# Kernel optimization log

Measured on AMD Instinct MI355X. Metric: run time of the kernel, lower is better.

Reference implementation:

```python
import jax, jax.numpy as jnp
import numpy as np

N = 512  # DFT size, fixed by the module


def _dft_weights():
    # W[h, j] = exp(-2i*pi*j*h/N), same as the torch init loop
    h = np.arange(N).reshape(N, 1).astype(np.float64)
    j = np.arange(N).reshape(1, N).astype(np.float64)
    ang = -2.0 * np.pi * (h * j) / N
    return np.cos(ang).astype(np.float32), np.sin(ang).astype(np.float32)


def setup_inputs() -> dict:
    key = jax.random.key(0)
    k1, k2 = jax.random.split(key)
    shape = (8, 16, 256, N)  # (batch, channels, doppler, range_samples)
    x_re = jax.random.normal(k1, shape, dtype=jnp.float32)
    x_im = jax.random.normal(k2, shape, dtype=jnp.float32)
    w_re, w_im = _dft_weights()
    return {
        "x_re": x_re,
        "x_im": x_im,
        "w_re": jnp.asarray(w_re),
        "w_im": jnp.asarray(w_im),
    }


def reference(x_re, x_im, w_re, w_im):
    # CplxLinear without bias: y = x @ W^T, complex.
    # y_re = x_re @ Wr^T - x_im @ Wi^T ; y_im = x_re @ Wi^T + x_im @ Wr^T
    y_re = jnp.einsum('bcdj,hj->bcdh', x_re, w_re) - jnp.einsum('bcdj,hj->bcdh', x_im, w_im)
    y_im = jnp.einsum('bcdj,hj->bcdh', x_re, w_im) + jnp.einsum('bcdj,hj->bcdh', x_im, w_re)
    # stack real/imag on trailing axis (equivalent to torch.view_as_real layout)
    return jnp.stack([y_re, y_im], axis=-1)
```

## Files before the change

### kernel.cpp

```cpp
#include <hip/hip_runtime.h>

typedef __bf16 bf16_t;
typedef __bf16 bf16x8 __attribute__((ext_vector_type(8)));
typedef float f32x4 __attribute__((ext_vector_type(4)));
typedef unsigned int u32x4 __attribute__((ext_vector_type(4)));

#define KDIM 512
#define NDIM 512
#define BM 128
#define BN 128
#define BK 32

__device__ __forceinline__ void gld_lds16(const float* g, float* lds_uniform) {
  __builtin_amdgcn_global_load_lds(
      (const __attribute__((address_space(1))) void*)g,
      (__attribute__((address_space(3))) void*)lds_uniform, 16, 0, 0);
}

__device__ __forceinline__ bf16x8 neg8(bf16x8 v) {
  union { bf16x8 b; u32x4 u; } x;
  x.b = v;
  x.u = x.u ^ 0x80008000u;
  return x.b;
}

__device__ __forceinline__ bf16x8 afrag(const float* ldsx, int r, int h4) {
  const int base = r * 8;
  const int sw = r & 7;
  const float4 a = *(const float4*)(ldsx + 4 * (base + ((2 * h4) ^ sw)));
  const float4 b = *(const float4*)(ldsx + 4 * (base + ((2 * h4 + 1) ^ sw)));
  bf16x8 f;
  f[0] = (__bf16)a.x; f[1] = (__bf16)a.y; f[2] = (__bf16)a.z; f[3] = (__bf16)a.w;
  f[4] = (__bf16)b.x; f[5] = (__bf16)b.y; f[6] = (__bf16)b.z; f[7] = (__bf16)b.w;
  return f;
}

__device__ __forceinline__ bf16x8 pack8(float4 a, float4 b) {
  bf16x8 f;
  f[0] = (__bf16)a.x; f[1] = (__bf16)a.y; f[2] = (__bf16)a.z; f[3] = (__bf16)a.w;
  f[4] = (__bf16)b.x; f[5] = (__bf16)b.y; f[6] = (__bf16)b.z; f[7] = (__bf16)b.w;
  return f;
}

__global__ __launch_bounds__(256, 2) void dft_cgemm_kernel(
    const float* __restrict__ xr, const float* __restrict__ xi,
    const float* __restrict__ wre, const float* __restrict__ wim,
    float* __restrict__ out) {
  __shared__ __align__(16) float lds_xr[BM * BK];
  __shared__ __align__(16) float lds_xi[BM * BK];
  __shared__ __align__(16) bf16_t lds_wr[BN * BK];
  __shared__ __align__(16) bf16_t lds_wi[BN * BK];

  const int t = threadIdx.x;
  const int lane = t & 63;
  const int wv = t >> 6;

  const int b = blockIdx.x;
  const int xcd = b & 7;
  const int sidx = b >> 3;
  const int m0 = (xcd * 32 + (sidx >> 2)) * BM;
  const int n0 = (sidx & 3) * BN;

  const int wm = (wv >> 1) * 64;
  const int wn = (wv & 1) * 64;
  const int l16 = lane & 15;
  const int h4 = lane >> 4;

  const int wt15 = t & 15;
  const int wg = (t >> 4) & 3;

  f32x4 acc_re[4][4], acc_im[4][4];
#pragma unroll
  for (int i = 0; i < 4; ++i)
#pragma unroll
    for (int j = 0; j < 4; ++j) {
      acc_re[i][j] = (f32x4){0.f, 0.f, 0.f, 0.f};
      acc_im[i][j] = (f32x4){0.f, 0.f, 0.f, 0.f};
    }

  for (int k0 = 0; k0 < KDIM; k0 += BK) {
#pragma unroll
    for (int it = 0; it < 4; ++it) {
      const int S = it * 256 + t;
      const int row = S >> 3;
      const int g = (S & 7) ^ (row & 7);
      const size_t goff = (size_t)(m0 + row) * KDIM + k0 + g * 4;
      float* dst_r = lds_xr + 4 * (it * 256 + wv * 64);
      float* dst_i = lds_xi + 4 * (it * 256 + wv * 64);
      gld_lds16(xr + goff, dst_r);
      gld_lds16(xi + goff, dst_i);
    }
#pragma unroll
    for (int c = 0; c < 2; ++c) {
      const int row = (c * 4 + wv) * 16 + wt15;
      const float* gr = wre + (size_t)(n0 + row) * KDIM + k0 + wg * 8;
      const float* gi = wim + (size_t)(n0 + row) * KDIM + k0 + wg * 8;
      const float4 r0 = ((const float4*)gr)[0];
      const float4 r1 = ((const float4*)gr)[1];
      const float4 i0 = ((const float4*)gi)[0];
      const float4 i1 = ((const float4*)gi)[1];
      const int slot = c * 256 + t;
      *(bf16x8*)(lds_wr + slot * 8) = pack8(r0, r1);
      *(bf16x8*)(lds_wi + slot * 8) = pack8(i0, i1);
    }
    __syncthreads();

    bf16x8 ar[4], ai[4], br[4], bi[4], nbi[4];
#pragma unroll
    for (int mi = 0; mi < 4; ++mi) {
      const int r = wm + mi * 16 + l16;
      ar[mi] = afrag(lds_xr, r, h4);
      ai[mi] = afrag(lds_xi, r, h4);
    }
#pragma unroll
    for (int ni = 0; ni < 4; ++ni) {
      const int slot = ((wn >> 4) + ni) * 64 + h4 * 16 + l16;
      br[ni] = *(const bf16x8*)(lds_wr + slot * 8);
      bi[ni] = *(const bf16x8*)(lds_wi + slot * 8);
      nbi[ni] = neg8(bi[ni]);
    }
#pragma unroll
    for (int mi = 0; mi < 4; ++mi) {
#pragma unroll
      for (int ni = 0; ni < 4; ++ni) {
        acc_re[mi][ni] = __builtin_amdgcn_mfma_f32_16x16x32_bf16(ar[mi], br[ni], acc_re[mi][ni], 0, 0, 0);
        acc_im[mi][ni] = __builtin_amdgcn_mfma_f32_16x16x32_bf16(ar[mi], bi[ni], acc_im[mi][ni], 0, 0, 0);
        acc_re[mi][ni] = __builtin_amdgcn_mfma_f32_16x16x32_bf16(ai[mi], nbi[ni], acc_re[mi][ni], 0, 0, 0);
        acc_im[mi][ni] = __builtin_amdgcn_mfma_f32_16x16x32_bf16(ai[mi], br[ni], acc_im[mi][ni], 0, 0, 0);
      }
    }
    __syncthreads();
  }

#pragma unroll
  for (int mi = 0; mi < 4; ++mi) {
#pragma unroll
    for (int r = 0; r < 4; ++r) {
      const int m = m0 + wm + mi * 16 + h4 * 4 + r;
#pragma unroll
      for (int ni = 0; ni < 4; ++ni) {
        const int h = n0 + wn + ni * 16 + l16;
        float2 v;
        v.x = acc_re[mi][ni][r];
        v.y = acc_im[mi][ni][r];
        *(float2*)(out + ((size_t)m * NDIM + h) * 2) = v;
      }
    }
  }
}

extern "C" void kernel_launch(void* const* d_in, const int* in_sizes, int n_in,
                              void* d_out, int out_size, void* d_ws, size_t ws_size,
                              hipStream_t stream) {
  const float* xr  = (const float*)d_in[0];
  const float* xi  = (const float*)d_in[1];
  const float* wre = (const float*)d_in[2];
  const float* wim = (const float*)d_in[3];
  float* out = (float*)d_out;

  dim3 grid(1024);
  dim3 block(256);
  dft_cgemm_kernel<<<grid, block, 0, stream>>>(xr, xi, wre, wim, out);
}
```

Baseline: 291.5 us.

## Double-buffer X tiles in LDS and prefetch W into registers

Makes the X tile in LDS double-buffered and issues the async global-to-LDS loads for the next K step before the MFMA work on the current one. The next W tile is also prefetched into registers so global latency overlaps compute, and the negation moves from B fragments onto A fragments. It costs twice the X LDS footprint, which could limit the two-blocks-per-CU target, plus extra registers for the W prefetch.

New measurement: 307.5 us. +5.5%, slower.

```diff
diff --git a/kernel.cpp b/kernel.cpp
--- a/kernel.cpp
+++ b/kernel.cpp
@@ -46,8 +46,7 @@
     const float* __restrict__ xr, const float* __restrict__ xi,
     const float* __restrict__ wre, const float* __restrict__ wim,
     float* __restrict__ out) {
-  __shared__ __align__(16) float lds_xr[BM * BK];
-  __shared__ __align__(16) float lds_xi[BM * BK];
+  __shared__ __align__(16) float lds_x[2][2][BM * BK];
   __shared__ __align__(16) bf16_t lds_wr[BN * BK];
   __shared__ __align__(16) bf16_t lds_wi[BN * BK];
 
@@ -66,8 +65,27 @@
   const int l16 = lane & 15;
   const int h4 = lane >> 4;
 
+  size_t goffx[4];
+  int dofx[4];
+#pragma unroll
+  for (int it = 0; it < 4; ++it) {
+    const int S = it * 256 + t;
+    const int row = S >> 3;
+    const int g = (S & 7) ^ (row & 7);
+    goffx[it] = (size_t)(m0 + row) * KDIM + g * 4;
+    dofx[it] = 4 * (it * 256 + wv * 64);
+  }
+
   const int wt15 = t & 15;
   const int wg = (t >> 4) & 3;
+  const float* gwr[2];
+  const float* gwi[2];
+#pragma unroll
+  for (int c = 0; c < 2; ++c) {
+    const int row = (c * 4 + wv) * 16 + wt15;
+    gwr[c] = wre + (size_t)(n0 + row) * KDIM + wg * 8;
+    gwi[c] = wim + (size_t)(n0 + row) * KDIM + wg * 8;
+  }
 
   f32x4 acc_re[4][4], acc_im[4][4];
 #pragma unroll
@@ -78,58 +96,75 @@
       acc_im[i][j] = (f32x4){0.f, 0.f, 0.f, 0.f};
     }
 
-  for (int k0 = 0; k0 < KDIM; k0 += BK) {
+  float4 wreg[8];
 #pragma unroll
-    for (int it = 0; it < 4; ++it) {
-      const int S = it * 256 + t;
-      const int row = S >> 3;
-      const int g = (S & 7) ^ (row & 7);
-      const size_t goff = (size_t)(m0 + row) * KDIM + k0 + g * 4;
-      float* dst_r = lds_xr + 4 * (it * 256 + wv * 64);
-      float* dst_i = lds_xi + 4 * (it * 256 + wv * 64);
-      gld_lds16(xr + goff, dst_r);
-      gld_lds16(xi + goff, dst_i);
-    }
+  for (int c = 0; c < 2; ++c) {
+    wreg[c * 4 + 0] = ((const float4*)(gwr[c]))[0];
+    wreg[c * 4 + 1] = ((const float4*)(gwr[c]))[1];
+    wreg[c * 4 + 2] = ((const float4*)(gwi[c]))[0];
+    wreg[c * 4 + 3] = ((const float4*)(gwi[c]))[1];
+  }
+#pragma unroll
+  for (int it = 0; it < 4; ++it) {
+    gld_lds16(xr + goffx[it], &lds_x[0][0][dofx[it]]);
+    gld_lds16(xi + goffx[it], &lds_x[0][1][dofx[it]]);
+  }
+
+  int cur = 0;
+  for (int k0 = 0; k0 < KDIM; k0 += BK, cur ^= 1) {
+    __syncthreads();
+
 #pragma unroll
     for (int c = 0; c < 2; ++c) {
-      const int row = (c * 4 + wv) * 16 + wt15;
-      const float* gr = wre + (size_t)(n0 + row) * KDIM + k0 + wg * 8;
-      const float* gi = wim + (size_t)(n0 + row) * KDIM + k0 + wg * 8;
-      const float4 r0 = ((const float4*)gr)[0];
-      const float4 r1 = ((const float4*)gr)[1];
-      const float4 i0 = ((const float4*)gi)[0];
-      const float4 i1 = ((const float4*)gi)[1];
       const int slot = c * 256 + t;
-      *(bf16x8*)(lds_wr + slot * 8) = pack8(r0, r1);
-      *(bf16x8*)(lds_wi + slot * 8) = pack8(i0, i1);
+      *(bf16x8*)(lds_wr + slot * 8) = pack8(wreg[c * 4 + 0], wreg[c * 4 + 1]);
+      *(bf16x8*)(lds_wi + slot * 8) = pack8(wreg[c * 4 + 2], wreg[c * 4 + 3]);
     }
     __syncthreads();
 
-    bf16x8 ar[4], ai[4], br[4], bi[4], nbi[4];
+    const int kn = k0 + BK;
+    if (kn < KDIM) {
+#pragma unroll
+      for (int it = 0; it < 4; ++it) {
+        gld_lds16(xr + goffx[it] + kn, &lds_x[cur ^ 1][0][dofx[it]]);
+        gld_lds16(xi + goffx[it] + kn, &lds_x[cur ^ 1][1][dofx[it]]);
+      }
+#pragma unroll
+      for (int c = 0; c < 2; ++c) {
+        wreg[c * 4 + 0] = ((const float4*)(gwr[c] + kn))[0];
+        wreg[c * 4 + 1] = ((const float4*)(gwr[c] + kn))[1];
+        wreg[c * 4 + 2] = ((const float4*)(gwi[c] + kn))[0];
+        wreg[c * 4 + 3] = ((const float4*)(gwi[c] + kn))[1];
+      }
+    }
+
+    const float* ldsxr = lds_x[cur][0];
+    const float* ldsxi = lds_x[cur][1];
+    bf16x8 ar[4], ai[4], br[4], bi[4];
 #pragma unroll
     for (int mi = 0; mi < 4; ++mi) {
       const int r = wm + mi * 16 + l16;
-      ar[mi] = afrag(lds_xr, r, h4);
-      ai[mi] = afrag(lds_xi, r, h4);
+      ar[mi] = afrag(ldsxr, r, h4);
+      ai[mi] = afrag(ldsxi, r, h4);
     }
 #pragma unroll
     for (int ni = 0; ni < 4; ++ni) {
       const int slot = ((wn >> 4) + ni) * 64 + h4 * 16 + l16;
       br[ni] = *(const bf16x8*)(lds_wr + slot * 8);
       bi[ni] = *(const bf16x8*)(lds_wi + slot * 8);
-      nbi[ni] = neg8(bi[ni]);
     }
+
 #pragma unroll
     for (int mi = 0; mi < 4; ++mi) {
+      const bf16x8 nai = neg8(ai[mi]);
 #pragma unroll
       for (int ni = 0; ni < 4; ++ni) {
         acc_re[mi][ni] = __builtin_amdgcn_mfma_f32_16x16x32_bf16(ar[mi], br[ni], acc_re[mi][ni], 0, 0, 0);
         acc_im[mi][ni] = __builtin_amdgcn_mfma_f32_16x16x32_bf16(ar[mi], bi[ni], acc_im[mi][ni], 0, 0, 0);
-        acc_re[mi][ni] = __builtin_amdgcn_mfma_f32_16x16x32_bf16(ai[mi], nbi[ni], acc_re[mi][ni], 0, 0, 0);
+        acc_re[mi][ni] = __builtin_amdgcn_mfma_f32_16x16x32_bf16(nai,    bi[ni], acc_re[mi][ni], 0, 0, 0);
         acc_im[mi][ni] = __builtin_amdgcn_mfma_f32_16x16x32_bf16(ai[mi], br[ni], acc_im[mi][ni], 0, 0, 0);
       }
     }
-    __syncthreads();
   }
 
 #pragma unroll
```
